# Kernel tuning notes

Hardware: AMD Instinct MI355X
Metric: run time of the kernel (lower is better)

Reference implementation:

```python
import jax, jax.numpy as jnp
import numpy as np

BINS = 64
MARGIN = 0.4


def setup_inputs() -> dict:
    key = jax.random.key(0)
    k1, k2 = jax.random.split(key)
    shape = (4, 2, 384, 384)  # [B, C, H, W] gradient-magnitude maps
    pred_grad = jax.random.uniform(k1, shape, dtype=jnp.float32)
    gt_grad = jax.random.uniform(k2, shape, dtype=jnp.float32)
    return {"pred_grad": pred_grad, "gt_grad": gt_grad}


def _soft_hist(mag, edges, bin_width):
    # triangular (linear interpolation) weights: only 1-2 bins nonzero per element
    w = jnp.clip(1.0 - jnp.abs(mag[..., None] - edges[:-1]) / bin_width, 0.0, 1.0)
    h = w.sum(axis=(0, 1, 2))  # sum over C, H, W -> [bins]
    return h / h.sum()


def reference(pred_grad, gt_grad):
    bin_weight = jnp.exp(MARGIN * jnp.arange(BINS, dtype=jnp.float32) / BINS)

    def per_sample(p_mag, g_mag):
        # dynamic bin range from 95th percentile of gt magnitudes;
        # torch uses .item() so bins are constants w.r.t. autograd -> stop_gradient
        max_val = jax.lax.stop_gradient(jnp.quantile(g_mag, 0.95))
        edges = jnp.arange(BINS + 1, dtype=jnp.float32) * (max_val / BINS)  # linspace(0, max, bins+1)
        bin_width = edges[1] - edges[0]
        p_hist = _soft_hist(p_mag, edges, bin_width)
        g_hist = _soft_hist(g_mag, edges, bin_width)
        return jnp.mean(jnp.abs(p_hist * bin_weight - g_hist * bin_weight))

    losses = jax.vmap(per_sample)(pred_grad, gt_grad)
    return losses.mean()  # sum over batch / len == mean
```

## Files before the change

### kernel.cpp

```cpp
#include <hip/hip_runtime.h>

#define SAMPLES 4
#define N 294912
#define NB 64
#define FB 2048
#define FBINW (1.0f / 2048.0f)
#define R0 280165
#define POISON 0xAAAAAAAAu

typedef float fx4 __attribute__((ext_vector_type(4)));

__device__ __forceinline__ int vbinf(float v) {
    int b = (int)(v * 2048.0f);
    return b < 0 ? 0 : (b > FB - 1 ? FB - 1 : b);
}

__global__ __launch_bounds__(256) void k_fused(const float* __restrict__ pred,
                                               const float* __restrict__ gt,
                                               unsigned* __restrict__ partial,
                                               unsigned* __restrict__ Lbits,
                                               unsigned* __restrict__ done,
                                               float* __restrict__ out) {
    int b = blockIdx.x, t = threadIdx.x;
    int m = b >> 4, p = b & 15, s = m & 3;
    __shared__ __align__(16) unsigned H2[FB / 2];
    __shared__ __align__(16) unsigned Hg[FB];
    __shared__ __align__(16) unsigned Hp[FB];
    __shared__ float sv[2];
    __shared__ double gnorm[NB];
    __shared__ unsigned tick_s;
    __shared__ unsigned wsum[4];

    const float* basep = (m < 4) ? (gt + m * N) : (pred + (m - 4) * N);
    const fx4* src = (const fx4*)basep + p * 4608;
    fx4 vv[18];
    #pragma unroll
    for (int i = 0; i < 18; i++)
        vv[i] = __builtin_nontemporal_load(&src[i * 256 + t]);

    #pragma unroll
    for (int i = 0; i < FB / 2 / 256; i++) H2[i * 256 + t] = 0u;
    __syncthreads();

    #pragma unroll
    for (int i = 0; i < 18; i++) {
        fx4 v = vv[i];
        int b0 = vbinf(v.x), b1 = vbinf(v.y), b2 = vbinf(v.z), b3 = vbinf(v.w);
        atomicAdd(&H2[b0 >> 1], 1u << ((b0 & 1) << 4));
        atomicAdd(&H2[b1 >> 1], 1u << ((b1 & 1) << 4));
        atomicAdd(&H2[b2 >> 1], 1u << ((b2 & 1) << 4));
        atomicAdd(&H2[b3 >> 1], 1u << ((b3 & 1) << 4));
    }
    __syncthreads();

    {
        uint4 v = ((const uint4*)H2)[t];
        unsigned long long* dst = (unsigned long long*)(partial + b * 1024);
        unsigned long long w0 = ((unsigned long long)v.y << 32) | (unsigned long long)v.x;
        unsigned long long w1 = ((unsigned long long)v.w << 32) | (unsigned long long)v.z;
        __hip_atomic_store(&dst[2 * t],     w0, __ATOMIC_RELAXED, __HIP_MEMORY_SCOPE_AGENT);
        __hip_atomic_store(&dst[2 * t + 1], w1, __ATOMIC_RELAXED, __HIP_MEMORY_SCOPE_AGENT);
    }
    __syncthreads();
    if (t == 0) {
        unsigned expct = POISON;
        __hip_atomic_compare_exchange_strong(&done[s], &expct, 0u,
                                             __ATOMIC_RELAXED, __ATOMIC_RELAXED,
                                             __HIP_MEMORY_SCOPE_AGENT);
        tick_s = __hip_atomic_fetch_add(&done[s], 1u,
                                        __ATOMIC_RELAXED, __HIP_MEMORY_SCOPE_AGENT);
    }
    __syncthreads();
    if (tick_s != 31u) return;

    if (t == 0) {
        __hip_atomic_store(&done[s], 0u, __ATOMIC_RELAXED, __HIP_MEMORY_SCOPE_AGENT);
        __builtin_amdgcn_fence(__ATOMIC_ACQUIRE, "agent");
    }
    __syncthreads();

    unsigned g[8] = {0, 0, 0, 0, 0, 0, 0, 0};
    unsigned q[8] = {0, 0, 0, 0, 0, 0, 0, 0};
    {
        const uint4* pg = (const uint4*)(partial + (s * 16) * 1024);
        const uint4* pp = (const uint4*)(partial + ((4 + s) * 16) * 1024);
        #pragma unroll
        for (int sl = 0; sl < 16; sl++) {
            uint4 wg = pg[sl * 256 + t];
            uint4 wp = pp[sl * 256 + t];
            g[0] += wg.x & 0xFFFFu; g[1] += wg.x >> 16;
            g[2] += wg.y & 0xFFFFu; g[3] += wg.y >> 16;
            g[4] += wg.z & 0xFFFFu; g[5] += wg.z >> 16;
            g[6] += wg.w & 0xFFFFu; g[7] += wg.w >> 16;
            q[0] += wp.x & 0xFFFFu; q[1] += wp.x >> 16;
            q[2] += wp.y & 0xFFFFu; q[3] += wp.y >> 16;
            q[4] += wp.z & 0xFFFFu; q[5] += wp.z >> 16;
            q[6] += wp.w & 0xFFFFu; q[7] += wp.w >> 16;
        }
    }
    ((uint4*)Hg)[2 * t]     = make_uint4(g[0], g[1], g[2], g[3]);
    ((uint4*)Hg)[2 * t + 1] = make_uint4(g[4], g[5], g[6], g[7]);
    ((uint4*)Hp)[2 * t]     = make_uint4(q[0], q[1], q[2], q[3]);
    ((uint4*)Hp)[2 * t + 1] = make_uint4(q[4], q[5], q[6], q[7]);

    unsigned sum = 0;
    #pragma unroll
    for (int k = 0; k < 8; k++) sum += g[k];
    unsigned incl = sum;
    int lane = t & 63, w = t >> 6;
    #pragma unroll
    for (int d = 1; d < 64; d <<= 1) {
        unsigned v = __shfl_up(incl, (unsigned)d, 64);
        if (lane >= d) incl += v;
    }
    if (lane == 63) wsum[w] = incl;
    __syncthreads();
    unsigned woff = 0;
    for (int i = 0; i < w; i++) woff += wsum[i];
    incl += woff;
    {
        unsigned before = incl - sum;
        for (int k = 0; k < 2; k++) {
            unsigned r = R0 + k;
            if (sum > 0 && before <= r && r < incl) {
                unsigned c = before;
                #pragma unroll
                for (int bb = 0; bb < 8; bb++) {
                    if (r < c + g[bb]) {
                        int bin = t * 8 + bb;
                        sv[k] = ((float)bin + ((float)(r - c) + 0.5f) / (float)g[bb]) * FBINW;
                        break;
                    }
                    c += g[bb];
                }
            }
        }
    }
    __syncthreads();
    float maxv = sv[0] + 0.45f * (sv[1] - sv[0]);
    float inv  = 64.0f / maxv;
    float a    = inv * FBINW;

    int which = t >> 6, j = t & 63;
    float hval = 0.0f;
    if (t < 128) {
        const unsigned* Hm = which ? Hp : Hg;
        int i_lo = 0;
        if (j > 0) { i_lo = (int)((float)(j - 1) / a) - 2; if (i_lo < 0) i_lo = 0; }
        int i_hi = (int)((float)(j + 1) / a) + 2; if (i_hi > FB) i_hi = FB;
        for (int i = i_lo; i < i_hi; i++) {
            unsigned c = Hm[i];
            if (c) {
                float xc = ((float)i + 0.5f) * a;
                int j0 = (int)xc;
                if (j0 == j)          hval += (1.0f - (xc - (float)j0)) * (float)c;
                else if (j0 == j - 1) hval += (xc - (float)j0) * (float)c;
            }
        }
    }
    float tot = hval;
    for (int mm = 1; mm < 64; mm <<= 1) tot += __shfl_xor(tot, mm, 64);
    double wj  = exp(0.4 * (double)j / 64.0);
    double val = (tot > 0.f) ? (double)hval / (double)tot * wj : 0.0;
    if (t < 64) gnorm[j] = val;
    __syncthreads();
    if (t >= 64 && t < 128) {
        double d = fabs(val - gnorm[j]);
        for (int mm = 1; mm < 64; mm <<= 1) d += __shfl_xor(d, mm, 64);
        if (j == 0)
            __hip_atomic_store(&Lbits[s], __float_as_uint((float)(d * (1.0 / 64.0))),
                               __ATOMIC_RELAXED, __HIP_MEMORY_SCOPE_AGENT);
    }
    __syncthreads();
    if (t == 0) {
        unsigned expct = POISON;
        __hip_atomic_compare_exchange_strong(&done[7], &expct, 0u,
                                             __ATOMIC_RELAXED, __ATOMIC_RELAXED,
                                             __HIP_MEMORY_SCOPE_AGENT);
        tick_s = __hip_atomic_fetch_add(&done[7], 1u,
                                        __ATOMIC_RELAXED, __HIP_MEMORY_SCOPE_AGENT);
    }
    __syncthreads();
    if (tick_s == 3u && t < 64) {
        float Lv = 0.f;
        if (t < 4)
            Lv = __uint_as_float(__hip_atomic_load(&Lbits[t], __ATOMIC_RELAXED,
                                                   __HIP_MEMORY_SCOPE_AGENT));
        Lv += __shfl_xor(Lv, 1, 64);
        Lv += __shfl_xor(Lv, 2, 64);
        if (t == 0) {
            out[0] = Lv * 0.25f;
            __hip_atomic_store(&done[7], 0u, __ATOMIC_RELAXED, __HIP_MEMORY_SCOPE_AGENT);
        }
    }
}

extern "C" void kernel_launch(void* const* d_in, const int* in_sizes, int n_in,
                              void* d_out, int out_size, void* d_ws, size_t ws_size,
                              hipStream_t stream) {
    const float* pred = (const float*)d_in[0];
    const float* gt   = (const float*)d_in[1];
    float* out = (float*)d_out;

    unsigned* ws      = (unsigned*)d_ws;
    unsigned* partial = ws;
    unsigned* Lbits   = partial + 128 * 1024;
    unsigned* done    = Lbits + SAMPLES;

    k_fused<<<128, 256, 0, stream>>>(pred, gt, partial, Lbits, done, out);
}
```

Before: 73.87 us.

## Double grid to 256 blocks and use per-wave unpacked LDS histograms

```diff
diff --git a/kernel.cpp b/kernel.cpp
--- a/kernel.cpp
+++ b/kernel.cpp
@@ -22,8 +22,8 @@
                                                unsigned* __restrict__ done,
                                                float* __restrict__ out) {
     int b = blockIdx.x, t = threadIdx.x;
-    int m = b >> 4, p = b & 15, s = m & 3;
-    __shared__ __align__(16) unsigned H2[FB / 2];
+    int m = b >> 5, p = b & 31, s = m & 3;
+    __shared__ __align__(16) unsigned SH[4][FB];
     __shared__ __align__(16) unsigned Hg[FB];
     __shared__ __align__(16) unsigned Hp[FB];
     __shared__ float sv[2];
@@ -32,32 +32,43 @@
     __shared__ unsigned wsum[4];
 
     const float* basep = (m < 4) ? (gt + m * N) : (pred + (m - 4) * N);
-    const fx4* src = (const fx4*)basep + p * 4608;
-    fx4 vv[18];
-    #pragma unroll
-    for (int i = 0; i < 18; i++)
+    const fx4* src = (const fx4*)basep + p * 2304;
+    fx4 vv[9];
+    #pragma unroll
+    for (int i = 0; i < 9; i++)
         vv[i] = __builtin_nontemporal_load(&src[i * 256 + t]);
 
     #pragma unroll
-    for (int i = 0; i < FB / 2 / 256; i++) H2[i * 256 + t] = 0u;
-    __syncthreads();
-
-    #pragma unroll
-    for (int i = 0; i < 18; i++) {
+    for (int i = 0; i < 8; i++)
+        ((uint4*)SH)[i * 256 + t] = make_uint4(0u, 0u, 0u, 0u);
+    __syncthreads();
+
+    unsigned* mh = SH[t >> 6];
+    #pragma unroll
+    for (int i = 0; i < 9; i++) {
         fx4 v = vv[i];
-        int b0 = vbinf(v.x), b1 = vbinf(v.y), b2 = vbinf(v.z), b3 = vbinf(v.w);
-        atomicAdd(&H2[b0 >> 1], 1u << ((b0 & 1) << 4));
-        atomicAdd(&H2[b1 >> 1], 1u << ((b1 & 1) << 4));
-        atomicAdd(&H2[b2 >> 1], 1u << ((b2 & 1) << 4));
-        atomicAdd(&H2[b3 >> 1], 1u << ((b3 & 1) << 4));
-    }
-    __syncthreads();
+        atomicAdd(&mh[vbinf(v.x)], 1u);
+        atomicAdd(&mh[vbinf(v.y)], 1u);
+        atomicAdd(&mh[vbinf(v.z)], 1u);
+        atomicAdd(&mh[vbinf(v.w)], 1u);
+    }
+    __syncthreads();
+
+    unsigned hb[8] = {0, 0, 0, 0, 0, 0, 0, 0};
+    #pragma unroll
+    for (int w4 = 0; w4 < 4; w4++) {
+        uint4 x = ((const uint4*)SH[w4])[2 * t];
+        uint4 y = ((const uint4*)SH[w4])[2 * t + 1];
+        hb[0] += x.x; hb[1] += x.y; hb[2] += x.z; hb[3] += x.w;
+        hb[4] += y.x; hb[5] += y.y; hb[6] += y.z; hb[7] += y.w;
+    }
 
     {
-        uint4 v = ((const uint4*)H2)[t];
         unsigned long long* dst = (unsigned long long*)(partial + b * 1024);
-        unsigned long long w0 = ((unsigned long long)v.y << 32) | (unsigned long long)v.x;
-        unsigned long long w1 = ((unsigned long long)v.w << 32) | (unsigned long long)v.z;
+        unsigned long long w0 = ((unsigned long long)(hb[2] | (hb[3] << 16)) << 32)
+                                | (unsigned long long)(hb[0] | (hb[1] << 16));
+        unsigned long long w1 = ((unsigned long long)(hb[6] | (hb[7] << 16)) << 32)
+                                | (unsigned long long)(hb[4] | (hb[5] << 16));
         __hip_atomic_store(&dst[2 * t],     w0, __ATOMIC_RELAXED, __HIP_MEMORY_SCOPE_AGENT);
         __hip_atomic_store(&dst[2 * t + 1], w1, __ATOMIC_RELAXED, __HIP_MEMORY_SCOPE_AGENT);
     }
@@ -71,7 +82,7 @@
                                         __ATOMIC_RELAXED, __HIP_MEMORY_SCOPE_AGENT);
     }
     __syncthreads();
-    if (tick_s != 31u) return;
+    if (tick_s != 63u) return;
 
     if (t == 0) {
         __hip_atomic_store(&done[s], 0u, __ATOMIC_RELAXED, __HIP_MEMORY_SCOPE_AGENT);
@@ -82,10 +93,10 @@
     unsigned g[8] = {0, 0, 0, 0, 0, 0, 0, 0};
     unsigned q[8] = {0, 0, 0, 0, 0, 0, 0, 0};
     {
-        const uint4* pg = (const uint4*)(partial + (s * 16) * 1024);
-        const uint4* pp = (const uint4*)(partial + ((4 + s) * 16) * 1024);
+        const uint4* pg = (const uint4*)(partial + (s * 32) * 1024);
+        const uint4* pp = (const uint4*)(partial + ((4 + s) * 32) * 1024);
         #pragma unroll
-        for (int sl = 0; sl < 16; sl++) {
+        for (int sl = 0; sl < 32; sl++) {
             uint4 wg = pg[sl * 256 + t];
             uint4 wp = pp[sl * 256 + t];
             g[0] += wg.x & 0xFFFFu; g[1] += wg.x >> 16;
@@ -204,8 +215,8 @@
 
     unsigned* ws      = (unsigned*)d_ws;
     unsigned* partial = ws;
-    unsigned* Lbits   = partial + 128 * 1024;
+    unsigned* Lbits   = partial + 256 * 1024;
     unsigned* done    = Lbits + SAMPLES;
 
-    k_fused<<<128, 256, 0, stream>>>(pred, gt, partial, Lbits, done, out);
+    k_fused<<<256, 256, 0, stream>>>(pred, gt, partial, Lbits, done, out);
 }
```

After: 79.88 us. +8.1%, slower.

## Split fused kernel into histogram and loss kernels to drop last-block sync

Applied to the files above, without the earlier changes.

```diff
diff --git a/kernel.cpp b/kernel.cpp
--- a/kernel.cpp
+++ b/kernel.cpp
@@ -15,21 +15,13 @@
     return b < 0 ? 0 : (b > FB - 1 ? FB - 1 : b);
 }
 
-__global__ __launch_bounds__(256) void k_fused(const float* __restrict__ pred,
-                                               const float* __restrict__ gt,
-                                               unsigned* __restrict__ partial,
-                                               unsigned* __restrict__ Lbits,
-                                               unsigned* __restrict__ done,
-                                               float* __restrict__ out) {
+
+__global__ __launch_bounds__(256) void k_hist(const float* __restrict__ pred,
+                                              const float* __restrict__ gt,
+                                              unsigned* __restrict__ partial) {
     int b = blockIdx.x, t = threadIdx.x;
-    int m = b >> 4, p = b & 15, s = m & 3;
+    int m = b >> 4, p = b & 15;
     __shared__ __align__(16) unsigned H2[FB / 2];
-    __shared__ __align__(16) unsigned Hg[FB];
-    __shared__ __align__(16) unsigned Hp[FB];
-    __shared__ float sv[2];
-    __shared__ double gnorm[NB];
-    __shared__ unsigned tick_s;
-    __shared__ unsigned wsum[4];
 
     const float* basep = (m < 4) ? (gt + m * N) : (pred + (m - 4) * N);
     const fx4* src = (const fx4*)basep + p * 4608;
@@ -53,31 +45,20 @@
     }
     __syncthreads();
 
-    {
-        uint4 v = ((const uint4*)H2)[t];
-        unsigned long long* dst = (unsigned long long*)(partial + b * 1024);
-        unsigned long long w0 = ((unsigned long long)v.y << 32) | (unsigned long long)v.x;
-        unsigned long long w1 = ((unsigned long long)v.w << 32) | (unsigned long long)v.z;
-        __hip_atomic_store(&dst[2 * t],     w0, __ATOMIC_RELAXED, __HIP_MEMORY_SCOPE_AGENT);
-        __hip_atomic_store(&dst[2 * t + 1], w1, __ATOMIC_RELAXED, __HIP_MEMORY_SCOPE_AGENT);
-    }
-    __syncthreads();
-    if (t == 0) {
-        unsigned expct = POISON;
-        __hip_atomic_compare_exchange_strong(&done[s], &expct, 0u,
-                                             __ATOMIC_RELAXED, __ATOMIC_RELAXED,
-                                             __HIP_MEMORY_SCOPE_AGENT);
-        tick_s = __hip_atomic_fetch_add(&done[s], 1u,
-                                        __ATOMIC_RELAXED, __HIP_MEMORY_SCOPE_AGENT);
-    }
-    __syncthreads();
-    if (tick_s != 31u) return;
+    ((uint4*)(partial + b * 1024))[t] = ((const uint4*)H2)[t];
+}
 
-    if (t == 0) {
-        __hip_atomic_store(&done[s], 0u, __ATOMIC_RELAXED, __HIP_MEMORY_SCOPE_AGENT);
-        __builtin_amdgcn_fence(__ATOMIC_ACQUIRE, "agent");
-    }
-    __syncthreads();
+__global__ __launch_bounds__(256) void k_loss(const unsigned* __restrict__ partial,
+                                              unsigned* __restrict__ Lbits,
+                                              unsigned* __restrict__ done,
+                                              float* __restrict__ out) {
+    int s = blockIdx.x, t = threadIdx.x;
+    __shared__ __align__(16) unsigned Hg[FB];
+    __shared__ __align__(16) unsigned Hp[FB];
+    __shared__ float sv[2];
+    __shared__ double gnorm[NB];
+    __shared__ unsigned tick_s;
+    __shared__ unsigned wsum[4];
 
     unsigned g[8] = {0, 0, 0, 0, 0, 0, 0, 0};
     unsigned q[8] = {0, 0, 0, 0, 0, 0, 0, 0};
@@ -207,5 +188,6 @@
     unsigned* Lbits   = partial + 128 * 1024;
     unsigned* done    = Lbits + SAMPLES;
 
-    k_fused<<<128, 256, 0, stream>>>(pred, gt, partial, Lbits, done, out);
+    k_hist<<<128, 256, 0, stream>>>(pred, gt, partial);
+    k_loss<<<SAMPLES, 256, 0, stream>>>(partial, Lbits, done, out);
 }
```

Result: no change. 72.75 us, median of 2 (-1.5%).
